# Kernel tuning notes

Measured on AMD Instinct MI355X. Metric: run time of the kernel, lower is better.

The kernel has to match this reference:

```python
import jax, jax.numpy as jnp
import numpy as np

H_HEADS = 8
DIM_HEAD = 64


def setup_inputs() -> dict:
    key = jax.random.key(0)
    ks = jax.random.split(key, 5)
    b, c, Hs, Ws = 16, 32, 128, 128
    qd = H_HEADS * c              # 256 (heads*c = Linear in_features)
    inner = H_HEADS * DIM_HEAD    # 512
    s = 0.02                      # keep logits in a sane range
    return {
        "x": jax.random.normal(ks[0], (b, c, Hs, Ws), jnp.float32),
        "Wq": jax.random.normal(ks[1], (inner, qd), jnp.float32) * s,
        "Wkv": jax.random.normal(ks[2], (2 * inner, qd), jnp.float32) * s,
        "Wout": jax.random.normal(ks[3], (qd, inner), jnp.float32) * s,
        "bout": jax.random.normal(ks[4], (qd,), jnp.float32) * s,
    }


def _proj(arg, W, bias=None):
    # apply_operator_or_ffn for nn.Linear:
    # rearrange '(b h) n d -> b d (h n)', Linear over last dim, then 'b d n -> b n d'
    B, n, d = arg.shape
    bp = B // H_HEADS
    t = arg.reshape(bp, H_HEADS, n, d)
    t = jnp.transpose(t, (0, 3, 1, 2)).reshape(bp, d, H_HEADS * n)  # [b', d, h*n]
    y = t @ W.T
    if bias is not None:
        y = y + bias
    return jnp.transpose(y, (0, 2, 1))  # [b', out_features, d]


def _split_heads(t):
    # 'b (h d) n -> (b h) d n'
    bp, hd, n = t.shape
    return t.reshape(bp, H_HEADS, hd // H_HEADS, n).reshape(bp * H_HEADS, hd // H_HEADS, n)


def reference(x, Wq, Wkv, Wout, bout):
    b, c = x.shape[0], x.shape[1]
    spatial = x.shape[2:]
    N = int(np.prod(spatial))
    scale = DIM_HEAD ** -0.5
    xf = x.reshape(b, c, N)
    q = _proj(xf, Wq)              # [b/h, inner, N]
    kv = _proj(xf, Wkv)            # [b/h, 2*inner, N]
    inner = q.shape[1]
    k, v = kv[:, :inner], kv[:, inner:]
    qh, kh, vh = _split_heads(q), _split_heads(k), _split_heads(v)  # [b, DIM_HEAD, N]
    sim = jnp.einsum('bin,bjn->bij', qh, kh) * scale                 # [b, dh, dh]
    attn = jax.nn.softmax(sim, axis=-1)
    out = jnp.einsum('bnj,bjd->bnd', attn, vh)                       # [b, dh, N]
    out = _proj(out, Wout, bout)                                     # [b/h, h*c, N]
    return out.reshape(b, c, *spatial)
```

## Files before the change

kernel.cpp:

```cpp
#include <hip/hip_runtime.h>
#include <cstdint>
#include <cstddef>

using u16 = unsigned short;
using u32 = unsigned int;

typedef __attribute__((ext_vector_type(8))) short bf16x8;
typedef __attribute__((ext_vector_type(16))) float f32x16;

__device__ __forceinline__ u16 f2bf(float f) {
  union { float f; u32 i; } x; x.f = f;
  u32 r = (x.i + 0x7FFFu + ((x.i >> 16) & 1u)) >> 16;
  return (u16)r;
}
__device__ __forceinline__ bf16x8 ldbf16x8(const u16* p) {
  union { uint4 u; bf16x8 v; } t;
  t.u = *(const uint4*)p;
  return t.v;
}

constexpr int NP = 16384;


constexpr size_t OFF_C   = 0;
constexpr size_t OFF_T   = 131072;
constexpr size_t OFF_AT  = 393216;
constexpr size_t OFF_WE  = 458752;
constexpr size_t OFF_MT  = 720896;
constexpr size_t OFF_MA  = 851968;
constexpr size_t OFF_XB  = 917504;
constexpr size_t OFF_XBT = 5111808;
constexpr size_t OFF_CP1 = 9306112;
constexpr size_t NEED1   = (OFF_CP1 + 4194304) * 4;
constexpr size_t OFF_CP2 = 851968;
constexpr size_t NEED2   = (OFF_CP2 + 6291456) * 4;

__global__ __launch_bounds__(256)
void k0_cvt(const float* __restrict__ x, u16* __restrict__ XbF,
            u16* __restrict__ XbTF) {
  __shared__ u32 Fs[256 * 33];
  const int pc = blockIdx.x;
  const int g  = blockIdx.y;
  const int p0 = pc * 64;
  const float* __restrict__ Xg = x + (size_t)g * 256 * NP;
  u16* __restrict__ XbFg  = XbF  + (size_t)g * 256 * NP;
  u16* __restrict__ XbTFg = XbTF + (size_t)g * NP * 256;
  const int tid = threadIdx.x;
  const int f8i = tid & 7, rb = tid >> 3;
  const int sA = pc * 4 + (f8i >> 1);
  const int hA = f8i & 1;
  for (int pass = 0; pass < 8; ++pass) {
    const int row = rb + pass * 32;
    const size_t e0 = (size_t)row * NP + p0 + f8i * 8;
    float4 a = *(const float4*)(Xg + e0);
    float4 b = *(const float4*)(Xg + e0 + 4);
    const float v[8] = {a.x, a.y, a.z, a.w, b.x, b.y, b.z, b.w};
    uint4 s;
    s.x = (u32)f2bf(v[0]) | ((u32)f2bf(v[1]) << 16);
    s.y = (u32)f2bf(v[2]) | ((u32)f2bf(v[3]) << 16);
    s.z = (u32)f2bf(v[4]) | ((u32)f2bf(v[5]) << 16);
    s.w = (u32)f2bf(v[6]) | ((u32)f2bf(v[7]) << 16);
    const int panel = row >> 5, lc = row & 31;
    *(uint4*)(XbFg + (size_t)panel * 524288 + sA * 512 + hA * 256 + lc * 8) = s;
    u32* d = &Fs[row * 33 + f8i * 4];
    d[0] = s.x; d[1] = s.y; d[2] = s.z; d[3] = s.w;
  }
  __syncthreads();
  const int p = tid & 63, grp = tid >> 6;
  const int pp = p0 + p;
  const int panelT = pp >> 5, lcT = pp & 31;
  const u16* __restrict__ Fs16 = (const u16*)Fs;
  u16* dstT = XbTFg + (size_t)panelT * 8192 + lcT * 8;
  for (int c = 0; c < 4; ++c) {
    const int sT = grp * 4 + c;
    u32 w[8];
#pragma unroll
    for (int q = 0; q < 8; ++q) {
      const int f = grp * 64 + c * 16 + q * 2;
      u32 lo = Fs16[f * 66 + p];
      u32 hi = Fs16[(f + 1) * 66 + p];
      w[q] = lo | (hi << 16);
    }
    uint4 s0 = {w[0], w[1], w[2], w[3]};
    uint4 s1 = {w[4], w[5], w[6], w[7]};
    *(uint4*)(dstT + sT * 512)       = s0;
    *(uint4*)(dstT + sT * 512 + 256) = s1;
  }
}

__global__ __launch_bounds__(256)
void k1_mfma(const u16* __restrict__ XbF, float* __restrict__ Cpart) {
  const int tp = blockIdx.x;
  const int kc = blockIdx.y;
  const int g  = blockIdx.z;
  const int ti = tp >> 1, tj = tp & 1;
  const int tid = threadIdx.x;
  const int w = tid >> 6, half = (tid >> 5) & 1, lc = tid & 31;
  const int qi = w >> 1, qj = w & 1;
  const u16* __restrict__ Xg = XbF + (size_t)g * 256 * NP;
  const size_t koff = (size_t)kc * 16384 + half * 256 + lc * 8;
  const u16* A0 = Xg + (size_t)(ti * 4 + qi * 2 + 0) * 524288 + koff;
  const u16* A1 = Xg + (size_t)(ti * 4 + qi * 2 + 1) * 524288 + koff;
  const u16* B0 = Xg + (size_t)(tj * 4 + qj * 2 + 0) * 524288 + koff;
  const u16* B1 = Xg + (size_t)(tj * 4 + qj * 2 + 1) * 524288 + koff;
  f32x16 acc00, acc01, acc10, acc11;
#pragma unroll
  for (int i = 0; i < 16; ++i) {
    acc00[i] = 0.f; acc01[i] = 0.f; acc10[i] = 0.f; acc11[i] = 0.f;
  }
#pragma unroll 4
  for (int s = 0; s < 32; ++s) {
    bf16x8 a0 = ldbf16x8(A0 + s * 512);
    bf16x8 a1 = ldbf16x8(A1 + s * 512);
    bf16x8 b0 = ldbf16x8(B0 + s * 512);
    bf16x8 b1 = ldbf16x8(B1 + s * 512);
    acc00 = __builtin_amdgcn_mfma_f32_32x32x16_bf16(a0, b0, acc00, 0, 0, 0);
    acc01 = __builtin_amdgcn_mfma_f32_32x32x16_bf16(a0, b1, acc01, 0, 0, 0);
    acc10 = __builtin_amdgcn_mfma_f32_32x32x16_bf16(a1, b0, acc10, 0, 0, 0);
    acc11 = __builtin_amdgcn_mfma_f32_32x32x16_bf16(a1, b1, acc11, 0, 0, 0);
  }
  float* __restrict__ P = Cpart + (((size_t)g * 4 + tp) * 32 + kc) * 16384;
#pragma unroll
  for (int r = 0; r < 16; ++r) {
    const int rr = (r & 3) + 8 * (r >> 2) + 4 * half;
    const int row0 = qi * 64 + rr, col0 = qj * 64 + lc;
    P[(row0 +  0) * 128 + col0 +  0] = acc00[r];
    P[(row0 +  0) * 128 + col0 + 32] = acc01[r];
    P[(row0 + 32) * 128 + col0 +  0] = acc10[r];
    P[(row0 + 32) * 128 + col0 + 32] = acc11[r];
  }
}

__global__ __launch_bounds__(256)
void k1b_red(const float* __restrict__ Cpart, float* __restrict__ Cmat) {
  const int sl = blockIdx.x;
  const int tp = blockIdx.y;
  const int g  = blockIdx.z;
  const int ele = sl * 256 + threadIdx.x;
  const float* __restrict__ P =
      Cpart + (((size_t)g * 4 + tp) * 32) * 16384 + ele;
  float v = 0.f;
#pragma unroll
  for (int kc = 0; kc < 32; ++kc) v += P[(size_t)kc * 16384];
  const int ti = tp >> 1, tj = tp & 1;
  const int i = ele >> 7, j = ele & 127;
  Cmat[(size_t)g * 65536 + (size_t)(ti * 128 + i) * 256 + tj * 128 + j] = v;
}

__global__ __launch_bounds__(256)
void k1_gram(const float* __restrict__ x, float* __restrict__ Cpart) {
  __shared__ float As[32 * 132];
  __shared__ float Bs[32 * 132];
  const int kc = blockIdx.x, ty = blockIdx.y, g = blockIdx.z;
  const int i0 = (ty == 2) ? 128 : 0;
  const int j0 = (ty == 0) ? 0 : 128;
  const float* __restrict__ Xg = x + (size_t)g * 256 * NP;
  const int tid = threadIdx.x, lane = tid & 63, w = tid >> 6;
  const int wy = (w >> 1) * 64, wx = (w & 1) * 64;
  const int ly = (lane >> 3) * 8, lx = (lane & 7) * 8;
  float acc[8][8];
#pragma unroll
  for (int e = 0; e < 8; ++e)
#pragma unroll
    for (int f = 0; f < 8; ++f) acc[e][f] = 0.f;
  const int k8 = (tid & 3) * 8, rowb = tid >> 2, k0 = kc * 256;
  for (int s = 0; s < 8; ++s) {
    const int ks = k0 + s * 32;
#pragma unroll
    for (int pass = 0; pass < 2; ++pass) {
      const int row = rowb + pass * 64;
      const size_t ea = (size_t)(i0 + row) * NP + ks + k8;
      float4 a = *(const float4*)(Xg + ea);
      float4 b = *(const float4*)(Xg + ea + 4);
      As[(k8+0)*132+row]=a.x; As[(k8+1)*132+row]=a.y;
      As[(k8+2)*132+row]=a.z; As[(k8+3)*132+row]=a.w;
      As[(k8+4)*132+row]=b.x; As[(k8+5)*132+row]=b.y;
      As[(k8+6)*132+row]=b.z; As[(k8+7)*132+row]=b.w;
      const size_t eb = (size_t)(j0 + row) * NP + ks + k8;
      a = *(const float4*)(Xg + eb);
      b = *(const float4*)(Xg + eb + 4);
      Bs[(k8+0)*132+row]=a.x; Bs[(k8+1)*132+row]=a.y;
      Bs[(k8+2)*132+row]=a.z; Bs[(k8+3)*132+row]=a.w;
      Bs[(k8+4)*132+row]=b.x; Bs[(k8+5)*132+row]=b.y;
      Bs[(k8+6)*132+row]=b.z; Bs[(k8+7)*132+row]=b.w;
    }
    __syncthreads();
#pragma unroll 4
    for (int kk = 0; kk < 32; ++kk) {
      const float* ar = &As[kk * 132 + wy + ly];
      const float* br = &Bs[kk * 132 + wx + lx];
      float4 a0 = *(const float4*)(ar), a1 = *(const float4*)(ar + 4);
      float4 b0 = *(const float4*)(br), b1 = *(const float4*)(br + 4);
      const float av[8] = {a0.x,a0.y,a0.z,a0.w,a1.x,a1.y,a1.z,a1.w};
      const float bv[8] = {b0.x,b0.y,b0.z,b0.w,b1.x,b1.y,b1.z,b1.w};
#pragma unroll
      for (int e = 0; e < 8; ++e)
#pragma unroll
        for (int f = 0; f < 8; ++f) acc[e][f] += av[e] * bv[f];
    }
    __syncthreads();
  }
  float* __restrict__ P = Cpart + (((size_t)g * 3 + ty) * 64 + kc) * 16384;
#pragma unroll
  for (int e = 0; e < 8; ++e) {
    float* pr = P + (size_t)(wy + ly + e) * 128 + wx + lx;
    float4 s0 = {acc[e][0], acc[e][1], acc[e][2], acc[e][3]};
    float4 s1 = {acc[e][4], acc[e][5], acc[e][6], acc[e][7]};
    *(float4*)(pr)     = s0;
    *(float4*)(pr + 4) = s1;
  }
}

__global__ __launch_bounds__(256)
void k1b_reduce(const float* __restrict__ Cpart, float* __restrict__ Cmat) {
  const int sl = blockIdx.x, ty = blockIdx.y, g = blockIdx.z;
  const int ele = sl * 256 + threadIdx.x;
  const float* __restrict__ P =
      Cpart + (((size_t)g * 3 + ty) * 64) * 16384 + ele;
  float v = 0.f;
#pragma unroll 8
  for (int kc = 0; kc < 64; ++kc) v += P[(size_t)kc * 16384];
  const int i0 = (ty == 2) ? 128 : 0;
  const int j0 = (ty == 0) ? 0 : 128;
  const int i = ele >> 7, j = ele & 127;
  float* Cg = Cmat + (size_t)g * 65536;
  Cg[(size_t)(i0 + i) * 256 + (j0 + j)] = v;
  if (ty == 1) Cg[(size_t)(j0 + j) * 256 + (i0 + i)] = v;
}

__global__ __launch_bounds__(256)
void k1_gram_atomic(const float* __restrict__ x, float* __restrict__ Cmat) {
  __shared__ float As[32 * 132];
  __shared__ float Bs[32 * 132];
  const int kc = blockIdx.x, ty = blockIdx.y, g = blockIdx.z;
  const int i0 = (ty == 2) ? 128 : 0;
  const int j0 = (ty == 0) ? 0 : 128;
  const float* __restrict__ Xg = x + (size_t)g * 256 * NP;
  const int tid = threadIdx.x, lane = tid & 63, w = tid >> 6;
  const int wy = (w >> 1) * 64, wx = (w & 1) * 64;
  const int ly = (lane >> 3) * 8, lx = (lane & 7) * 8;
  float acc[8][8];
#pragma unroll
  for (int e = 0; e < 8; ++e)
#pragma unroll
    for (int f = 0; f < 8; ++f) acc[e][f] = 0.f;
  const int k8 = (tid & 3) * 8, rowb = tid >> 2, k0 = kc * 256;
  for (int s = 0; s < 8; ++s) {
    const int ks = k0 + s * 32;
#pragma unroll
    for (int pass = 0; pass < 2; ++pass) {
      const int row = rowb + pass * 64;
      const size_t ea = (size_t)(i0 + row) * NP + ks + k8;
      float4 a = *(const float4*)(Xg + ea);
      float4 b = *(const float4*)(Xg + ea + 4);
      As[(k8+0)*132+row]=a.x; As[(k8+1)*132+row]=a.y;
      As[(k8+2)*132+row]=a.z; As[(k8+3)*132+row]=a.w;
      As[(k8+4)*132+row]=b.x; As[(k8+5)*132+row]=b.y;
      As[(k8+6)*132+row]=b.z; As[(k8+7)*132+row]=b.w;
      const size_t eb = (size_t)(j0 + row) * NP + ks + k8;
      a = *(const float4*)(Xg + eb);
      b = *(const float4*)(Xg + eb + 4);
      Bs[(k8+0)*132+row]=a.x; Bs[(k8+1)*132+row]=a.y;
      Bs[(k8+2)*132+row]=a.z; Bs[(k8+3)*132+row]=a.w;
      Bs[(k8+4)*132+row]=b.x; Bs[(k8+5)*132+row]=b.y;
      Bs[(k8+6)*132+row]=b.z; Bs[(k8+7)*132+row]=b.w;
    }
    __syncthreads();
#pragma unroll 4
    for (int kk = 0; kk < 32; ++kk) {
      const float* ar = &As[kk * 132 + wy + ly];
      const float* br = &Bs[kk * 132 + wx + lx];
      float4 a0 = *(const float4*)(ar), a1 = *(const float4*)(ar + 4);
      float4 b0 = *(const float4*)(br), b1 = *(const float4*)(br + 4);
      const float av[8] = {a0.x,a0.y,a0.z,a0.w,a1.x,a1.y,a1.z,a1.w};
      const float bv[8] = {b0.x,b0.y,b0.z,b0.w,b1.x,b1.y,b1.z,b1.w};
#pragma unroll
      for (int e = 0; e < 8; ++e)
#pragma unroll
        for (int f = 0; f < 8; ++f) acc[e][f] += av[e] * bv[f];
    }
    __syncthreads();
  }
  float* Cg = Cmat + (size_t)g * 65536;
#pragma unroll
  for (int e = 0; e < 8; ++e)
#pragma unroll
    for (int f = 0; f < 8; ++f) {
      atomicAdd(&Cg[(i0+wy+ly+e)*256 + (j0+wx+lx+f)], acc[e][f]);
      if (ty == 1)
        atomicAdd(&Cg[(j0+wx+lx+f)*256 + (i0+wy+ly+e)], acc[e][f]);
    }
}

__global__ __launch_bounds__(256)
void kA_attn(const float* __restrict__ Wq, const float* __restrict__ Wkv,
             const float* __restrict__ Cmat, float* __restrict__ attn) {
  __shared__ float WqL[4 * 256];
  __shared__ float Ts[4 * 256];
  const int bh = blockIdx.x;
  const int ic = blockIdx.y;
  const int g = bh >> 3, hh = bh & 7;
  const int tid = threadIdx.x;
  const float* __restrict__ Cg = Cmat + (size_t)g * 65536;
  {
    const int r = tid >> 6, c4 = (tid & 63) * 4;
    *(float4*)(&WqL[r * 256 + c4]) =
        *(const float4*)(Wq + (size_t)(hh * 64 + ic * 4 + r) * 256 + c4);
  }
  __syncthreads();
  float acc[4] = {0.f, 0.f, 0.f, 0.f};
#pragma unroll 8
  for (int b = 0; b < 256; ++b) {
    const float cv = Cg[(size_t)b * 256 + tid];
#pragma unroll
    for (int r = 0; r < 4; ++r) acc[r] += WqL[r * 256 + b] * cv;
  }
#pragma unroll
  for (int r = 0; r < 4; ++r) Ts[r * 256 + tid] = acc[r];
  __syncthreads();
  const int r = tid >> 6, j = tid & 63;
  const float* __restrict__ Wk = Wkv + (size_t)(hh * 64 + j) * 256;
  float s = 0.f;
#pragma unroll 4
  for (int a4 = 0; a4 < 64; ++a4) {
    float4 w = *(const float4*)(Wk + a4 * 4);
    const float* t4 = &Ts[r * 256 + a4 * 4];
    s += t4[0] * w.x + t4[1] * w.y + t4[2] * w.z + t4[3] * w.w;
  }
  s *= 0.125f;
  float m = s;
#pragma unroll
  for (int off = 32; off; off >>= 1) m = fmaxf(m, __shfl_xor(m, off));
  const float e = __expf(s - m);
  float sum = e;
#pragma unroll
  for (int off = 32; off; off >>= 1) sum += __shfl_xor(sum, off);
  attn[((size_t)bh * 64 + ic * 4 + r) * 64 + j] = e / sum;
}

__global__ __launch_bounds__(256)
void kB_m(const float* __restrict__ Wout, const float* __restrict__ Wkv,
          const float* __restrict__ attn, float* __restrict__ Mp) {
  __shared__ float AtL[64 * 64];
  __shared__ float WoL[16 * 64];
  __shared__ float UL[16 * 64];
  const int bh = blockIdx.x;
  const int cc = blockIdx.y;
  const int g = bh >> 3, hh = bh & 7;
  const int tid = threadIdx.x;
  {
    const float* __restrict__ A = attn + (size_t)bh * 4096;
#pragma unroll
    for (int q = 0; q < 4; ++q)
      *(float4*)(&AtL[q * 1024 + tid * 4]) =
          *(const float4*)(A + q * 1024 + tid * 4);
  }
  {
    const int co_l = tid >> 4, i4 = (tid & 15) * 4;
    *(float4*)(&WoL[co_l * 64 + i4]) =
        *(const float4*)(Wout + (size_t)(cc * 16 + co_l) * 512 + hh * 64 + i4);
  }
  __syncthreads();
  const int j = tid & 63, cw = tid >> 6;
  float u4[4] = {0.f, 0.f, 0.f, 0.f};
#pragma unroll 4
  for (int i = 0; i < 64; ++i) {
    const float av = AtL[i * 64 + j];
#pragma unroll
    for (int u = 0; u < 4; ++u) u4[u] += WoL[(cw * 4 + u) * 64 + i] * av;
  }
  __syncthreads();
#pragma unroll
  for (int u = 0; u < 4; ++u) UL[(cw * 4 + u) * 64 + j] = u4[u];
  __syncthreads();
  float acc[16];
#pragma unroll
  for (int c = 0; c < 16; ++c) acc[c] = 0.f;
#pragma unroll 4
  for (int j2 = 0; j2 < 64; ++j2) {
    const float wv = Wkv[(size_t)(512 + hh * 64 + j2) * 256 + tid];
#pragma unroll
    for (int c = 0; c < 16; ++c) acc[c] += UL[c * 64 + j2] * wv;
  }
  float* __restrict__ P =
      Mp + (((size_t)g * 8 + hh) * 256 + cc * 16) * 256 + tid;
#pragma unroll
  for (int c = 0; c < 16; ++c) P[(size_t)c * 256] = acc[c];
}

__global__ __launch_bounds__(256)
void kC_red(const float* __restrict__ Mp, u16* __restrict__ MA) {
  const int panel = blockIdx.x >> 2;
  const int q     = blockIdx.x & 3;
  const int g     = blockIdx.y;
  const int tid = threadIdx.x;
  const float* __restrict__ Pg = Mp + (size_t)g * 8 * 65536;
  u16* __restrict__ Mg = MA + (size_t)g * 65536;
  const int item = tid + q * 256;
  const int lc = item & 31;
  const int co = panel * 32 + lc;
  const int b0 = (item >> 5) * 8;
  float v[8] = {0.f, 0.f, 0.f, 0.f, 0.f, 0.f, 0.f, 0.f};
#pragma unroll
  for (int hd = 0; hd < 8; ++hd) {
    const float* p = Pg + (size_t)hd * 65536 + (size_t)co * 256 + b0;
    float4 a = *(const float4*)(p);
    float4 b = *(const float4*)(p + 4);
    v[0] += a.x; v[1] += a.y; v[2] += a.z; v[3] += a.w;
    v[4] += b.x; v[5] += b.y; v[6] += b.z; v[7] += b.w;
  }
  uint4 sdat;
  sdat.x = (u32)f2bf(v[0]) | ((u32)f2bf(v[1]) << 16);
  sdat.y = (u32)f2bf(v[2]) | ((u32)f2bf(v[3]) << 16);
  sdat.z = (u32)f2bf(v[4]) | ((u32)f2bf(v[5]) << 16);
  sdat.w = (u32)f2bf(v[6]) | ((u32)f2bf(v[7]) << 16);
  *(uint4*)(Mg + (size_t)panel * 8192 + (size_t)item * 8) = sdat;
}

__global__ __launch_bounds__(256) void k2_T(const float* __restrict__ Wq,
                                            const float* __restrict__ Cmat,
                                            float* __restrict__ T) {
  const int bh = blockIdx.x;
  const int ic = blockIdx.y;
  const int g = bh >> 3, hh = bh & 7;
  const int tid = threadIdx.x;
  const float* __restrict__ Cg = Cmat + (size_t)g * 65536;
  const int r0 = hh * 64 + ic * 4;
  float acc[4] = {0.f, 0.f, 0.f, 0.f};
#pragma unroll 8
  for (int b = 0; b < 256; ++b) {
    const float cv = Cg[(size_t)b * 256 + tid];
#pragma unroll
    for (int ii = 0; ii < 4; ++ii)
      acc[ii] += Wq[(size_t)(r0 + ii) * 256 + b] * cv;
  }
#pragma unroll
  for (int ii = 0; ii < 4; ++ii)
    T[((size_t)bh * 64 + ic * 4 + ii) * 256 + tid] = acc[ii];
}

__global__ __launch_bounds__(256) void k3_sim(const float* __restrict__ Wkv,
                                              const float* __restrict__ T,
                                              float* __restrict__ simattn) {
  __shared__ float Ts[64 * 256];
  const int bh = blockIdx.x;
  const int jc = blockIdx.y;
  const int hh = bh & 7;
  const int tid = threadIdx.x;
  {
    const int f4i = tid & 63;
    const int rwb = tid >> 6;
    for (int pass = 0; pass < 16; ++pass) {
      const int row = rwb + pass * 4;
      float4 v = *(const float4*)(T + ((size_t)bh * 64 + row) * 256 + f4i * 4);
      const int a0 = f4i * 4;
      const float vv[4] = {v.x, v.y, v.z, v.w};
#pragma unroll
      for (int e = 0; e < 4; ++e) {
        const int a = a0 + e;
        Ts[row * 256 + (a & ~31) + ((a + row) & 31)] = vv[e];
      }
    }
  }
  __syncthreads();
  const int i  = tid & 63;
  const int jq = tid >> 6;
  const int jb = jc * 16 + jq * 4;
  float acc[4] = {0.f, 0.f, 0.f, 0.f};
#pragma unroll 4
  for (int a = 0; a < 256; ++a) {
    const float tv = Ts[i * 256 + (a & ~31) + ((a + i) & 31)];
#pragma unroll
    for (int jj = 0; jj < 4; ++jj)
      acc[jj] += Wkv[(size_t)(hh * 64 + jb + jj) * 256 + a] * tv;
  }
#pragma unroll
  for (int jj = 0; jj < 4; ++jj)
    simattn[((size_t)bh * 64 + i) * 64 + jb + jj] = acc[jj] * 0.125f;
}

__global__ __launch_bounds__(64) void k3b_softmax(float* __restrict__ simattn) {
  const int bh = blockIdx.x;
  const int i  = threadIdx.x;
  float* row = simattn + ((size_t)bh * 64 + i) * 64;
  float v[64];
  float m = -1e30f;
#pragma unroll
  for (int j = 0; j < 64; ++j) { v[j] = row[j]; m = fmaxf(m, v[j]); }
  float s = 0.f;
#pragma unroll
  for (int j = 0; j < 64; ++j) { v[j] = __expf(v[j] - m); s += v[j]; }
  const float inv = 1.0f / s;
#pragma unroll
  for (int j = 0; j < 64; ++j) row[j] = v[j] * inv;
}

__global__ __launch_bounds__(256) void k4_we(const float* __restrict__ Wout,
                                             const float* __restrict__ attn,
                                             float* __restrict__ WeT) {
  __shared__ float WL[256 * 64];
  const int jc = blockIdx.x;
  const int hh = blockIdx.y;
  const int g  = blockIdx.z;
  const int bh = g * 8 + hh;
  const int tid = threadIdx.x;
  {
    const int f4i = tid & 15;
    const int cb  = tid >> 4;
    for (int pass = 0; pass < 16; ++pass) {
      const int co = cb + pass * 16;
      float4 v = *(const float4*)(Wout + (size_t)co * 512 + hh * 64 + f4i * 4);
      const int a0 = f4i * 4;
      const float vv[4] = {v.x, v.y, v.z, v.w};
#pragma unroll
      for (int e = 0; e < 4; ++e)
        WL[co * 64 + ((a0 + e + co) & 63)] = vv[e];
    }
  }
  __syncthreads();
  const int jb = jc * 8;
  float acc[8] = {0.f, 0.f, 0.f, 0.f, 0.f, 0.f, 0.f, 0.f};
#pragma unroll 4
  for (int i = 0; i < 64; ++i) {
    const float wv = WL[tid * 64 + ((i + tid) & 63)];
#pragma unroll
    for (int je = 0; je < 8; ++je)
      acc[je] += attn[((size_t)bh * 64 + i) * 64 + jb + je] * wv;
  }
#pragma unroll
  for (int je = 0; je < 8; ++je)
    WeT[(size_t)g * 131072 + (size_t)(hh * 64 + jb + je) * 256 + tid] =
        acc[je];
}

__global__ __launch_bounds__(256)
void k5a_part(const float* __restrict__ Wkv, const float* __restrict__ WeT,
              float* __restrict__ Mp) {
  const int bc = blockIdx.x;
  const int oc = blockIdx.y;
  const int g  = blockIdx.z;
  const int tid = threadIdx.x;
  const int b0 = bc * 4;
  const float* __restrict__ Weg = WeT + (size_t)g * 131072;
  float acc[4] = {0.f, 0.f, 0.f, 0.f};
#pragma unroll 8
  for (int u = 0; u < 32; ++u) {
    const int o = oc * 32 + u;
    const float wv = Weg[(size_t)o * 256 + tid];
    const float* __restrict__ vr = Wkv + (size_t)(512 + o) * 256 + b0;
    acc[0] += vr[0] * wv;
    acc[1] += vr[1] * wv;
    acc[2] += vr[2] * wv;
    acc[3] += vr[3] * wv;
  }
#pragma unroll
  for (int be = 0; be < 4; ++be)
    Mp[(((size_t)g * 16 + oc) * 256 + b0 + be) * 256 + tid] = acc[be];
}

__global__ __launch_bounds__(256)
void k5b_red(const float* __restrict__ Mp, float* __restrict__ Mt,
             u16* __restrict__ MA) {
  const int b = blockIdx.x;
  const int g = blockIdx.y;
  const int tid = threadIdx.x;
  const float* __restrict__ P =
      Mp + ((size_t)g * 16 * 256 + b) * 256 + tid;
  float v = 0.f;
#pragma unroll
  for (int oc = 0; oc < 16; ++oc) v += P[(size_t)oc * 65536];
  Mt[(size_t)g * 65536 + (size_t)b * 256 + tid] = v;
  MA[(size_t)g * 65536 + (size_t)tid * 256 + b] = f2bf(v);
}

__global__ __launch_bounds__(256) void k5_serial(const float* __restrict__ Wkv,
                                                 const float* __restrict__ WeT,
                                                 float* __restrict__ Mt,
                                                 u16* __restrict__ MA) {
  const int bc = blockIdx.x;
  const int g  = blockIdx.y;
  const int tid = threadIdx.x;
  const int b0 = bc * 4;
  const float* __restrict__ Weg = WeT + (size_t)g * 131072;
  float acc[4] = {0.f, 0.f, 0.f, 0.f};
#pragma unroll 4
  for (int o = 0; o < 512; ++o) {
    const float wv = Weg[(size_t)o * 256 + tid];
    const float* __restrict__ vr = Wkv + (size_t)(512 + o) * 256 + b0;
    acc[0] += vr[0] * wv;
    acc[1] += vr[1] * wv;
    acc[2] += vr[2] * wv;
    acc[3] += vr[3] * wv;
  }
#pragma unroll
  for (int be = 0; be < 4; ++be) {
    Mt[(size_t)g * 65536 + (size_t)(b0 + be) * 256 + tid] = acc[be];
    MA[(size_t)g * 65536 + (size_t)tid * 256 + b0 + be] = f2bf(acc[be]);
  }
}

__global__ __launch_bounds__(256)
void k6_mfma(const u16* __restrict__ XbTF, const u16* __restrict__ MA,
             const float* __restrict__ bout, float* __restrict__ out) {
  const int pb = blockIdx.x;
  const int cb = blockIdx.y;
  const int g  = blockIdx.z;
  const int tid = threadIdx.x;
  const int w = tid >> 6, half = (tid >> 5) & 1, lc = tid & 31;
  const int p0  = pb * 128 + w * 32;
  const int co0 = cb * 128;
  const u16* __restrict__ Ap = XbTF + (size_t)g * NP * 256 +
                               (size_t)(pb * 4 + w) * 8192 + half * 256 +
                               lc * 8;
  const u16* __restrict__ Bp = MA + (size_t)g * 65536 +
                               (size_t)cb * 32768 + half * 256 + lc * 8;
  f32x16 acc[4];
#pragma unroll
  for (int t = 0; t < 4; ++t)
#pragma unroll
    for (int i = 0; i < 16; ++i) acc[t][i] = 0.f;
#pragma unroll 2
  for (int s = 0; s < 16; ++s) {
    bf16x8 a = ldbf16x8(Ap + s * 512);
#pragma unroll
    for (int t = 0; t < 4; ++t) {
      bf16x8 b = ldbf16x8(Bp + (size_t)t * 8192 + s * 512);
      acc[t] = __builtin_amdgcn_mfma_f32_32x32x16_bf16(a, b, acc[t], 0, 0, 0);
    }
  }
#pragma unroll
  for (int t = 0; t < 4; ++t) {
    const int co = co0 + t * 32 + lc;
    const float bo = bout[co];
    float* __restrict__ ocol =
        out + ((size_t)(g * 256 + co)) * NP + p0 + 4 * half;
#pragma unroll
    for (int rg = 0; rg < 4; ++rg) {
      float4 v = {acc[t][rg * 4 + 0] + bo, acc[t][rg * 4 + 1] + bo,
                  acc[t][rg * 4 + 2] + bo, acc[t][rg * 4 + 3] + bo};
      *(float4*)(ocol + rg * 8) = v;
    }
  }
}

__global__ __launch_bounds__(256)
void k6_apply(const float* __restrict__ x, const float* __restrict__ Mt,
              const float* __restrict__ bout, float* __restrict__ out) {
  __shared__ float As[32 * 132];
  __shared__ float Bs[32 * 132];
  const int pc = blockIdx.x;
  const int oy = blockIdx.y;
  const int g  = blockIdx.z;
  const int p0 = pc * 128;
  const int o0 = oy * 128;
  const float* __restrict__ Xg = x + (size_t)g * 256 * NP;
  const float* __restrict__ Mg = Mt + (size_t)g * 65536;
  const int tid  = threadIdx.x;
  const int lane = tid & 63;
  const int w    = tid >> 6;
  const int wy = (w >> 1) * 64;
  const int wx = (w & 1) * 64;
  const int ly = (lane >> 3) * 8;
  const int lx = (lane & 7) * 8;
  float acc[8][8];
#pragma unroll
  for (int e = 0; e < 8; ++e)
#pragma unroll
    for (int f = 0; f < 8; ++f) acc[e][f] = 0.f;
  const int c4 = (tid & 31) * 4;
  const int kb = tid >> 5;
  for (int s = 0; s < 8; ++s) {
#pragma unroll
    for (int r = 0; r < 4; ++r) {
      const int kk = kb + r * 8;
      const int f  = s * 32 + kk;
      *(float4*)&As[kk * 132 + c4] =
          *(const float4*)(Mg + (size_t)f * 256 + o0 + c4);
      *(float4*)&Bs[kk * 132 + c4] =
          *(const float4*)(Xg + (size_t)f * NP + p0 + c4);
    }
    __syncthreads();
#pragma unroll 4
    for (int kk = 0; kk < 32; ++kk) {
      const float* __restrict__ ar = &As[kk * 132 + wy + ly];
      const float* __restrict__ br = &Bs[kk * 132 + wx + lx];
      float4 a0 = *(const float4*)(ar);
      float4 a1 = *(const float4*)(ar + 4);
      float4 b0 = *(const float4*)(br);
      float4 b1 = *(const float4*)(br + 4);
      const float av[8] = {a0.x, a0.y, a0.z, a0.w, a1.x, a1.y, a1.z, a1.w};
      const float bv[8] = {b0.x, b0.y, b0.z, b0.w, b1.x, b1.y, b1.z, b1.w};
#pragma unroll
      for (int e = 0; e < 8; ++e)
#pragma unroll
        for (int f = 0; f < 8; ++f) acc[e][f] += av[e] * bv[f];
    }
    __syncthreads();
  }
#pragma unroll
  for (int e = 0; e < 8; ++e) {
    const int co = o0 + wy + ly + e;
    const float bo = bout[co];
    float* __restrict__ orow =
        out + ((size_t)(g * 256 + co)) * NP + p0 + wx + lx;
    float4 s0 = {acc[e][0] + bo, acc[e][1] + bo, acc[e][2] + bo,
                 acc[e][3] + bo};
    float4 s1 = {acc[e][4] + bo, acc[e][5] + bo, acc[e][6] + bo,
                 acc[e][7] + bo};
    *(float4*)(orow)     = s0;
    *(float4*)(orow + 4) = s1;
  }
}

extern "C" void kernel_launch(void* const* d_in, const int* in_sizes, int n_in,
                              void* d_out, int out_size, void* d_ws,
                              size_t ws_size, hipStream_t stream) {
  const float* x    = (const float*)d_in[0];
  const float* Wq   = (const float*)d_in[1];
  const float* Wkv  = (const float*)d_in[2];
  const float* Wout = (const float*)d_in[3];
  const float* bout = (const float*)d_in[4];
  float* out = (float*)d_out;
  float* ws  = (float*)d_ws;

  float* C    = ws + OFF_C;
  float* T    = ws + OFF_T;
  float* att  = ws + OFF_AT;
  float* WeT  = ws + OFF_WE;
  float* Mt   = ws + OFF_MT;
  u16*   MA   = (u16*)(ws + OFF_MA);
  u16*   Xb   = (u16*)(ws + OFF_XB);
  u16*   XbT  = (u16*)(ws + OFF_XBT);
  float* Cp1  = ws + OFF_CP1;
  float* Cp2  = ws + OFF_CP2;

  const bool mfma_path = (ws_size >= NEED1);
  const bool splitk    = (ws_size >= NEED2);

  if (mfma_path) {
    k0_cvt<<<dim3(256, 2), 256, 0, stream>>>(x, Xb, XbT);
    k1_mfma<<<dim3(4, 32, 2), 256, 0, stream>>>(Xb, Cp1);
    k1b_red<<<dim3(64, 4, 2), 256, 0, stream>>>(Cp1, C);
    kA_attn<<<dim3(16, 16), 256, 0, stream>>>(Wq, Wkv, C, att);
    kB_m<<<dim3(16, 16), 256, 0, stream>>>(Wout, Wkv, att, Cp1);
    kC_red<<<dim3(32, 2), 256, 0, stream>>>(Cp1, MA);
    k6_mfma<<<dim3(128, 2, 2), 256, 0, stream>>>(XbT, MA, bout, out);
    return;
  }

  if (splitk) {
    k1_gram<<<dim3(64, 3, 2), 256, 0, stream>>>(x, Cp2);
    k1b_reduce<<<dim3(64, 3, 2), 256, 0, stream>>>(Cp2, C);
  } else {
    hipMemsetAsync(C, 0, 131072 * sizeof(float), stream);
    k1_gram_atomic<<<dim3(64, 3, 2), 256, 0, stream>>>(x, C);
  }
  k2_T<<<dim3(16, 16), 256, 0, stream>>>(Wq, C, T);
  k3_sim<<<dim3(16, 4), 256, 0, stream>>>(Wkv, T, att);
  k3b_softmax<<<dim3(16), 64, 0, stream>>>(att);
  k4_we<<<dim3(8, 8, 2), 256, 0, stream>>>(Wout, att, WeT);
  if (splitk) {
    k5a_part<<<dim3(64, 16, 2), 256, 0, stream>>>(Wkv, WeT, Cp2);
    k5b_red<<<dim3(256, 2), 256, 0, stream>>>(Cp2, Mt, MA);
  } else {
    k5_serial<<<dim3(64, 2), 256, 0, stream>>>(Wkv, WeT, Mt, MA);
  }
  k6_apply<<<dim3(128, 2, 2), 256, 0, stream>>>(x, Mt, bout, out);
}
```

Baseline: 159.3 us.

## Drop transposed bf16 copy of x; transpose in LDS inside final GEMM

The conversion kernel no longer writes a second, transposed bf16 copy of x. The final MFMA kernel instead loads its 128-pixel slice from the feature-major bf16 buffer and transposes it into padded shared memory before the MFMAs. This removes one full write of the bf16 tensor and shrinks the workspace. In exchange, the output kernel now does scattered 16-bit LDS stores and needs a block barrier, and each of the two channel blocks repeats the transpose.

```diff
diff --git a/kernel.cpp b/kernel.cpp
--- a/kernel.cpp
+++ b/kernel.cpp
@@ -29,62 +29,35 @@
 constexpr size_t OFF_MT  = 720896;
 constexpr size_t OFF_MA  = 851968;
 constexpr size_t OFF_XB  = 917504;
-constexpr size_t OFF_XBT = 5111808;
-constexpr size_t OFF_CP1 = 9306112;
+constexpr size_t OFF_CP1 = 5111808;
 constexpr size_t NEED1   = (OFF_CP1 + 4194304) * 4;
 constexpr size_t OFF_CP2 = 851968;
 constexpr size_t NEED2   = (OFF_CP2 + 6291456) * 4;
 
 __global__ __launch_bounds__(256)
-void k0_cvt(const float* __restrict__ x, u16* __restrict__ XbF,
-            u16* __restrict__ XbTF) {
-  __shared__ u32 Fs[256 * 33];
+void k0_cvt(const float* __restrict__ x, u16* __restrict__ XbF) {
   const int pc = blockIdx.x;
   const int g  = blockIdx.y;
   const int p0 = pc * 64;
   const float* __restrict__ Xg = x + (size_t)g * 256 * NP;
-  u16* __restrict__ XbFg  = XbF  + (size_t)g * 256 * NP;
-  u16* __restrict__ XbTFg = XbTF + (size_t)g * NP * 256;
+  u16* __restrict__ XbFg = XbF + (size_t)g * 256 * NP;
   const int tid = threadIdx.x;
   const int f8i = tid & 7, rb = tid >> 3;
   const int sA = pc * 4 + (f8i >> 1);
   const int hA = f8i & 1;
+#pragma unroll
   for (int pass = 0; pass < 8; ++pass) {
     const int row = rb + pass * 32;
     const size_t e0 = (size_t)row * NP + p0 + f8i * 8;
     float4 a = *(const float4*)(Xg + e0);
     float4 b = *(const float4*)(Xg + e0 + 4);
-    const float v[8] = {a.x, a.y, a.z, a.w, b.x, b.y, b.z, b.w};
     uint4 s;
-    s.x = (u32)f2bf(v[0]) | ((u32)f2bf(v[1]) << 16);
-    s.y = (u32)f2bf(v[2]) | ((u32)f2bf(v[3]) << 16);
-    s.z = (u32)f2bf(v[4]) | ((u32)f2bf(v[5]) << 16);
-    s.w = (u32)f2bf(v[6]) | ((u32)f2bf(v[7]) << 16);
+    s.x = (u32)f2bf(a.x) | ((u32)f2bf(a.y) << 16);
+    s.y = (u32)f2bf(a.z) | ((u32)f2bf(a.w) << 16);
+    s.z = (u32)f2bf(b.x) | ((u32)f2bf(b.y) << 16);
+    s.w = (u32)f2bf(b.z) | ((u32)f2bf(b.w) << 16);
     const int panel = row >> 5, lc = row & 31;
     *(uint4*)(XbFg + (size_t)panel * 524288 + sA * 512 + hA * 256 + lc * 8) = s;
-    u32* d = &Fs[row * 33 + f8i * 4];
-    d[0] = s.x; d[1] = s.y; d[2] = s.z; d[3] = s.w;
-  }
-  __syncthreads();
-  const int p = tid & 63, grp = tid >> 6;
-  const int pp = p0 + p;
-  const int panelT = pp >> 5, lcT = pp & 31;
-  const u16* __restrict__ Fs16 = (const u16*)Fs;
-  u16* dstT = XbTFg + (size_t)panelT * 8192 + lcT * 8;
-  for (int c = 0; c < 4; ++c) {
-    const int sT = grp * 4 + c;
-    u32 w[8];
-#pragma unroll
-    for (int q = 0; q < 8; ++q) {
-      const int f = grp * 64 + c * 16 + q * 2;
-      u32 lo = Fs16[f * 66 + p];
-      u32 hi = Fs16[(f + 1) * 66 + p];
-      w[q] = lo | (hi << 16);
-    }
-    uint4 s0 = {w[0], w[1], w[2], w[3]};
-    uint4 s1 = {w[4], w[5], w[6], w[7]};
-    *(uint4*)(dstT + sT * 512)       = s0;
-    *(uint4*)(dstT + sT * 512 + 256) = s1;
   }
 }
 
@@ -145,6 +118,191 @@
   const int ti = tp >> 1, tj = tp & 1;
   const int i = ele >> 7, j = ele & 127;
   Cmat[(size_t)g * 65536 + (size_t)(ti * 128 + i) * 256 + tj * 128 + j] = v;
+}
+
+__global__ __launch_bounds__(256)
+void kA_attn(const float* __restrict__ Wq, const float* __restrict__ Wkv,
+             const float* __restrict__ Cmat, float* __restrict__ attn) {
+  __shared__ float WqL[4 * 256];
+  __shared__ float Ts[4 * 256];
+  const int bh = blockIdx.x;
+  const int ic = blockIdx.y;
+  const int g = bh >> 3, hh = bh & 7;
+  const int tid = threadIdx.x;
+  const float* __restrict__ Cg = Cmat + (size_t)g * 65536;
+  {
+    const int r = tid >> 6, c4 = (tid & 63) * 4;
+    *(float4*)(&WqL[r * 256 + c4]) =
+        *(const float4*)(Wq + (size_t)(hh * 64 + ic * 4 + r) * 256 + c4);
+  }
+  __syncthreads();
+  float acc[4] = {0.f, 0.f, 0.f, 0.f};
+#pragma unroll 8
+  for (int b = 0; b < 256; ++b) {
+    const float cv = Cg[(size_t)b * 256 + tid];
+#pragma unroll
+    for (int r = 0; r < 4; ++r) acc[r] += WqL[r * 256 + b] * cv;
+  }
+#pragma unroll
+  for (int r = 0; r < 4; ++r) Ts[r * 256 + tid] = acc[r];
+  __syncthreads();
+  const int r = tid >> 6, j = tid & 63;
+  const float* __restrict__ Wk = Wkv + (size_t)(hh * 64 + j) * 256;
+  float s = 0.f;
+#pragma unroll 4
+  for (int a4 = 0; a4 < 64; ++a4) {
+    float4 w = *(const float4*)(Wk + a4 * 4);
+    const float* t4 = &Ts[r * 256 + a4 * 4];
+    s += t4[0] * w.x + t4[1] * w.y + t4[2] * w.z + t4[3] * w.w;
+  }
+  s *= 0.125f;
+  float m = s;
+#pragma unroll
+  for (int off = 32; off; off >>= 1) m = fmaxf(m, __shfl_xor(m, off));
+  const float e = __expf(s - m);
+  float sum = e;
+#pragma unroll
+  for (int off = 32; off; off >>= 1) sum += __shfl_xor(sum, off);
+  attn[((size_t)bh * 64 + ic * 4 + r) * 64 + j] = e / sum;
+}
+
+__global__ __launch_bounds__(256)
+void kB_m(const float* __restrict__ Wout, const float* __restrict__ Wkv,
+          const float* __restrict__ attn, float* __restrict__ Mp) {
+  __shared__ float AtL[64 * 64];
+  __shared__ float WoL[16 * 64];
+  __shared__ float UL[16 * 64];
+  const int bh = blockIdx.x;
+  const int cc = blockIdx.y;
+  const int g = bh >> 3, hh = bh & 7;
+  const int tid = threadIdx.x;
+  {
+    const float* __restrict__ A = attn + (size_t)bh * 4096;
+#pragma unroll
+    for (int q = 0; q < 4; ++q)
+      *(float4*)(&AtL[q * 1024 + tid * 4]) =
+          *(const float4*)(A + q * 1024 + tid * 4);
+  }
+  {
+    const int co_l = tid >> 4, i4 = (tid & 15) * 4;
+    *(float4*)(&WoL[co_l * 64 + i4]) =
+        *(const float4*)(Wout + (size_t)(cc * 16 + co_l) * 512 + hh * 64 + i4);
+  }
+  __syncthreads();
+  const int j = tid & 63, cw = tid >> 6;
+  float u4[4] = {0.f, 0.f, 0.f, 0.f};
+#pragma unroll 4
+  for (int i = 0; i < 64; ++i) {
+    const float av = AtL[i * 64 + j];
+#pragma unroll
+    for (int u = 0; u < 4; ++u) u4[u] += WoL[(cw * 4 + u) * 64 + i] * av;
+  }
+  __syncthreads();
+#pragma unroll
+  for (int u = 0; u < 4; ++u) UL[(cw * 4 + u) * 64 + j] = u4[u];
+  __syncthreads();
+  float acc[16];
+#pragma unroll
+  for (int c = 0; c < 16; ++c) acc[c] = 0.f;
+#pragma unroll 4
+  for (int j2 = 0; j2 < 64; ++j2) {
+    const float wv = Wkv[(size_t)(512 + hh * 64 + j2) * 256 + tid];
+#pragma unroll
+    for (int c = 0; c < 16; ++c) acc[c] += UL[c * 64 + j2] * wv;
+  }
+  float* __restrict__ P =
+      Mp + (((size_t)g * 8 + hh) * 256 + cc * 16) * 256 + tid;
+#pragma unroll
+  for (int c = 0; c < 16; ++c) P[(size_t)c * 256] = acc[c];
+}
+
+__global__ __launch_bounds__(256)
+void kC_red(const float* __restrict__ Mp, u16* __restrict__ MA) {
+  const int panel = blockIdx.x >> 2;
+  const int q     = blockIdx.x & 3;
+  const int g     = blockIdx.y;
+  const int tid = threadIdx.x;
+  const float* __restrict__ Pg = Mp + (size_t)g * 8 * 65536;
+  u16* __restrict__ Mg = MA + (size_t)g * 65536;
+  const int item = tid + q * 256;
+  const int lc = item & 31;
+  const int co = panel * 32 + lc;
+  const int b0 = (item >> 5) * 8;
+  float v[8] = {0.f, 0.f, 0.f, 0.f, 0.f, 0.f, 0.f, 0.f};
+#pragma unroll
+  for (int hd = 0; hd < 8; ++hd) {
+    const float* p = Pg + (size_t)hd * 65536 + (size_t)co * 256 + b0;
+    float4 a = *(const float4*)(p);
+    float4 b = *(const float4*)(p + 4);
+    v[0] += a.x; v[1] += a.y; v[2] += a.z; v[3] += a.w;
+    v[4] += b.x; v[5] += b.y; v[6] += b.z; v[7] += b.w;
+  }
+  uint4 sdat;
+  sdat.x = (u32)f2bf(v[0]) | ((u32)f2bf(v[1]) << 16);
+  sdat.y = (u32)f2bf(v[2]) | ((u32)f2bf(v[3]) << 16);
+  sdat.z = (u32)f2bf(v[4]) | ((u32)f2bf(v[5]) << 16);
+  sdat.w = (u32)f2bf(v[6]) | ((u32)f2bf(v[7]) << 16);
+  *(uint4*)(Mg + (size_t)panel * 8192 + (size_t)item * 8) = sdat;
+}
+
+__global__ __launch_bounds__(256)
+void k6_mfma(const u16* __restrict__ XbF, const u16* __restrict__ MA,
+             const float* __restrict__ bout, float* __restrict__ out) {
+  __shared__ u16 T[128 * 264];
+  const int pb = blockIdx.x;
+  const int cb = blockIdx.y;
+  const int g  = blockIdx.z;
+  const int tid = threadIdx.x;
+  const u16* __restrict__ Xg = XbF + (size_t)g * 256 * NP;
+  for (int it = 0; it < 16; ++it) {
+    const int idx = it * 256 + tid;
+    const int pa  = idx >> 9;
+    const int o2  = (idx & 511) * 8;
+    union { uint4 u; u16 e[8]; } v;
+    v.u = *(const uint4*)(Xg + (size_t)pa * 524288 + (size_t)pb * 4096 + o2);
+    const int sp_l = o2 >> 9;
+    const int r    = o2 & 511;
+    const int h    = r >> 8;
+    const int lcf  = (r >> 3) & 31;
+    const int f    = pa * 32 + lcf;
+    const int pl   = sp_l * 16 + h * 8;
+#pragma unroll
+    for (int jj = 0; jj < 8; ++jj) T[(pl + jj) * 264 + f] = v.e[jj];
+  }
+  __syncthreads();
+  const int w = tid >> 6, half = (tid >> 5) & 1, lc = tid & 31;
+  const int p0  = pb * 128 + w * 32;
+  const int co0 = cb * 128;
+  const u16* __restrict__ Ap = &T[(w * 32 + lc) * 264 + half * 8];
+  const u16* __restrict__ Bp = MA + (size_t)g * 65536 +
+                               (size_t)cb * 32768 + half * 256 + lc * 8;
+  f32x16 acc[4];
+#pragma unroll
+  for (int t = 0; t < 4; ++t)
+#pragma unroll
+    for (int i = 0; i < 16; ++i) acc[t][i] = 0.f;
+#pragma unroll 2
+  for (int s = 0; s < 16; ++s) {
+    bf16x8 a = ldbf16x8(Ap + s * 16);
+#pragma unroll
+    for (int t = 0; t < 4; ++t) {
+      bf16x8 b = ldbf16x8(Bp + (size_t)t * 8192 + s * 512);
+      acc[t] = __builtin_amdgcn_mfma_f32_32x32x16_bf16(a, b, acc[t], 0, 0, 0);
+    }
+  }
+#pragma unroll
+  for (int t = 0; t < 4; ++t) {
+    const int co = co0 + t * 32 + lc;
+    const float bo = bout[co];
+    float* __restrict__ ocol =
+        out + ((size_t)(g * 256 + co)) * NP + p0 + 4 * half;
+#pragma unroll
+    for (int rg = 0; rg < 4; ++rg) {
+      float4 v = {acc[t][rg * 4 + 0] + bo, acc[t][rg * 4 + 1] + bo,
+                  acc[t][rg * 4 + 2] + bo, acc[t][rg * 4 + 3] + bo};
+      *(float4*)(ocol + rg * 8) = v;
+    }
+  }
 }
 
 __global__ __launch_bounds__(256)
@@ -292,131 +450,6 @@
     }
 }
 
-__global__ __launch_bounds__(256)
-void kA_attn(const float* __restrict__ Wq, const float* __restrict__ Wkv,
-             const float* __restrict__ Cmat, float* __restrict__ attn) {
-  __shared__ float WqL[4 * 256];
-  __shared__ float Ts[4 * 256];
-  const int bh = blockIdx.x;
-  const int ic = blockIdx.y;
-  const int g = bh >> 3, hh = bh & 7;
-  const int tid = threadIdx.x;
-  const float* __restrict__ Cg = Cmat + (size_t)g * 65536;
-  {
-    const int r = tid >> 6, c4 = (tid & 63) * 4;
-    *(float4*)(&WqL[r * 256 + c4]) =
-        *(const float4*)(Wq + (size_t)(hh * 64 + ic * 4 + r) * 256 + c4);
-  }
-  __syncthreads();
-  float acc[4] = {0.f, 0.f, 0.f, 0.f};
-#pragma unroll 8
-  for (int b = 0; b < 256; ++b) {
-    const float cv = Cg[(size_t)b * 256 + tid];
-#pragma unroll
-    for (int r = 0; r < 4; ++r) acc[r] += WqL[r * 256 + b] * cv;
-  }
-#pragma unroll
-  for (int r = 0; r < 4; ++r) Ts[r * 256 + tid] = acc[r];
-  __syncthreads();
-  const int r = tid >> 6, j = tid & 63;
-  const float* __restrict__ Wk = Wkv + (size_t)(hh * 64 + j) * 256;
-  float s = 0.f;
-#pragma unroll 4
-  for (int a4 = 0; a4 < 64; ++a4) {
-    float4 w = *(const float4*)(Wk + a4 * 4);
-    const float* t4 = &Ts[r * 256 + a4 * 4];
-    s += t4[0] * w.x + t4[1] * w.y + t4[2] * w.z + t4[3] * w.w;
-  }
-  s *= 0.125f;
-  float m = s;
-#pragma unroll
-  for (int off = 32; off; off >>= 1) m = fmaxf(m, __shfl_xor(m, off));
-  const float e = __expf(s - m);
-  float sum = e;
-#pragma unroll
-  for (int off = 32; off; off >>= 1) sum += __shfl_xor(sum, off);
-  attn[((size_t)bh * 64 + ic * 4 + r) * 64 + j] = e / sum;
-}
-
-__global__ __launch_bounds__(256)
-void kB_m(const float* __restrict__ Wout, const float* __restrict__ Wkv,
-          const float* __restrict__ attn, float* __restrict__ Mp) {
-  __shared__ float AtL[64 * 64];
-  __shared__ float WoL[16 * 64];
-  __shared__ float UL[16 * 64];
-  const int bh = blockIdx.x;
-  const int cc = blockIdx.y;
-  const int g = bh >> 3, hh = bh & 7;
-  const int tid = threadIdx.x;
-  {
-    const float* __restrict__ A = attn + (size_t)bh * 4096;
-#pragma unroll
-    for (int q = 0; q < 4; ++q)
-      *(float4*)(&AtL[q * 1024 + tid * 4]) =
-          *(const float4*)(A + q * 1024 + tid * 4);
-  }
-  {
-    const int co_l = tid >> 4, i4 = (tid & 15) * 4;
-    *(float4*)(&WoL[co_l * 64 + i4]) =
-        *(const float4*)(Wout + (size_t)(cc * 16 + co_l) * 512 + hh * 64 + i4);
-  }
-  __syncthreads();
-  const int j = tid & 63, cw = tid >> 6;
-  float u4[4] = {0.f, 0.f, 0.f, 0.f};
-#pragma unroll 4
-  for (int i = 0; i < 64; ++i) {
-    const float av = AtL[i * 64 + j];
-#pragma unroll
-    for (int u = 0; u < 4; ++u) u4[u] += WoL[(cw * 4 + u) * 64 + i] * av;
-  }
-  __syncthreads();
-#pragma unroll
-  for (int u = 0; u < 4; ++u) UL[(cw * 4 + u) * 64 + j] = u4[u];
-  __syncthreads();
-  float acc[16];
-#pragma unroll
-  for (int c = 0; c < 16; ++c) acc[c] = 0.f;
-#pragma unroll 4
-  for (int j2 = 0; j2 < 64; ++j2) {
-    const float wv = Wkv[(size_t)(512 + hh * 64 + j2) * 256 + tid];
-#pragma unroll
-    for (int c = 0; c < 16; ++c) acc[c] += UL[c * 64 + j2] * wv;
-  }
-  float* __restrict__ P =
-      Mp + (((size_t)g * 8 + hh) * 256 + cc * 16) * 256 + tid;
-#pragma unroll
-  for (int c = 0; c < 16; ++c) P[(size_t)c * 256] = acc[c];
-}
-
-__global__ __launch_bounds__(256)
-void kC_red(const float* __restrict__ Mp, u16* __restrict__ MA) {
-  const int panel = blockIdx.x >> 2;
-  const int q     = blockIdx.x & 3;
-  const int g     = blockIdx.y;
-  const int tid = threadIdx.x;
-  const float* __restrict__ Pg = Mp + (size_t)g * 8 * 65536;
-  u16* __restrict__ Mg = MA + (size_t)g * 65536;
-  const int item = tid + q * 256;
-  const int lc = item & 31;
-  const int co = panel * 32 + lc;
-  const int b0 = (item >> 5) * 8;
-  float v[8] = {0.f, 0.f, 0.f, 0.f, 0.f, 0.f, 0.f, 0.f};
-#pragma unroll
-  for (int hd = 0; hd < 8; ++hd) {
-    const float* p = Pg + (size_t)hd * 65536 + (size_t)co * 256 + b0;
-    float4 a = *(const float4*)(p);
-    float4 b = *(const float4*)(p + 4);
-    v[0] += a.x; v[1] += a.y; v[2] += a.z; v[3] += a.w;
-    v[4] += b.x; v[5] += b.y; v[6] += b.z; v[7] += b.w;
-  }
-  uint4 sdat;
-  sdat.x = (u32)f2bf(v[0]) | ((u32)f2bf(v[1]) << 16);
-  sdat.y = (u32)f2bf(v[2]) | ((u32)f2bf(v[3]) << 16);
-  sdat.z = (u32)f2bf(v[4]) | ((u32)f2bf(v[5]) << 16);
-  sdat.w = (u32)f2bf(v[6]) | ((u32)f2bf(v[7]) << 16);
-  *(uint4*)(Mg + (size_t)panel * 8192 + (size_t)item * 8) = sdat;
-}
-
 __global__ __launch_bounds__(256) void k2_T(const float* __restrict__ Wq,
                                             const float* __restrict__ Cmat,
                                             float* __restrict__ T) {
@@ -596,50 +629,6 @@
   for (int be = 0; be < 4; ++be) {
     Mt[(size_t)g * 65536 + (size_t)(b0 + be) * 256 + tid] = acc[be];
     MA[(size_t)g * 65536 + (size_t)tid * 256 + b0 + be] = f2bf(acc[be]);
-  }
-}
-
-__global__ __launch_bounds__(256)
-void k6_mfma(const u16* __restrict__ XbTF, const u16* __restrict__ MA,
-             const float* __restrict__ bout, float* __restrict__ out) {
-  const int pb = blockIdx.x;
-  const int cb = blockIdx.y;
-  const int g  = blockIdx.z;
-  const int tid = threadIdx.x;
-  const int w = tid >> 6, half = (tid >> 5) & 1, lc = tid & 31;
-  const int p0  = pb * 128 + w * 32;
-  const int co0 = cb * 128;
-  const u16* __restrict__ Ap = XbTF + (size_t)g * NP * 256 +
-                               (size_t)(pb * 4 + w) * 8192 + half * 256 +
-                               lc * 8;
-  const u16* __restrict__ Bp = MA + (size_t)g * 65536 +
-                               (size_t)cb * 32768 + half * 256 + lc * 8;
-  f32x16 acc[4];
-#pragma unroll
-  for (int t = 0; t < 4; ++t)
-#pragma unroll
-    for (int i = 0; i < 16; ++i) acc[t][i] = 0.f;
-#pragma unroll 2
-  for (int s = 0; s < 16; ++s) {
-    bf16x8 a = ldbf16x8(Ap + s * 512);
-#pragma unroll
-    for (int t = 0; t < 4; ++t) {
-      bf16x8 b = ldbf16x8(Bp + (size_t)t * 8192 + s * 512);
-      acc[t] = __builtin_amdgcn_mfma_f32_32x32x16_bf16(a, b, acc[t], 0, 0, 0);
-    }
-  }
-#pragma unroll
-  for (int t = 0; t < 4; ++t) {
-    const int co = co0 + t * 32 + lc;
-    const float bo = bout[co];
-    float* __restrict__ ocol =
-        out + ((size_t)(g * 256 + co)) * NP + p0 + 4 * half;
-#pragma unroll
-    for (int rg = 0; rg < 4; ++rg) {
-      float4 v = {acc[t][rg * 4 + 0] + bo, acc[t][rg * 4 + 1] + bo,
-                  acc[t][rg * 4 + 2] + bo, acc[t][rg * 4 + 3] + bo};
-      *(float4*)(ocol + rg * 8) = v;
-    }
   }
 }
 
@@ -730,7 +719,6 @@
   float* Mt   = ws + OFF_MT;
   u16*   MA   = (u16*)(ws + OFF_MA);
   u16*   Xb   = (u16*)(ws + OFF_XB);
-  u16*   XbT  = (u16*)(ws + OFF_XBT);
   float* Cp1  = ws + OFF_CP1;
   float* Cp2  = ws + OFF_CP2;
 
@@ -738,13 +726,13 @@
   const bool splitk    = (ws_size >= NEED2);
 
   if (mfma_path) {
-    k0_cvt<<<dim3(256, 2), 256, 0, stream>>>(x, Xb, XbT);
+    k0_cvt<<<dim3(256, 2), 256, 0, stream>>>(x, Xb);
     k1_mfma<<<dim3(4, 32, 2), 256, 0, stream>>>(Xb, Cp1);
     k1b_red<<<dim3(64, 4, 2), 256, 0, stream>>>(Cp1, C);
     kA_attn<<<dim3(16, 16), 256, 0, stream>>>(Wq, Wkv, C, att);
     kB_m<<<dim3(16, 16), 256, 0, stream>>>(Wout, Wkv, att, Cp1);
     kC_red<<<dim3(32, 2), 256, 0, stream>>>(Cp1, MA);
-    k6_mfma<<<dim3(128, 2, 2), 256, 0, stream>>>(XbT, MA, bout, out);
+    k6_mfma<<<dim3(128, 2, 2), 256, 0, stream>>>(Xb, MA, bout, out);
     return;
   }
 
```

Measured after the change: 156.3 us. About the same (-1.8%).
